# Kernel tuning notes

Hardware: AMD Instinct MI355X
Metric: run time of the kernel (lower is better)

## Reference

```python
import jax, jax.numpy as jnp
import numpy as np

N = 50000      # nodes
E = 800000     # edges
D = 256        # hidden_dim (input node features)
A = 128        # attention_dim = attention_ratio * heads
H = 8          # heads
DK = A // H    # 16


def setup_inputs() -> dict:
    key = jax.random.key(0)
    ks = jax.random.split(key, 6)
    x = jax.random.normal(ks[0], (N, D), dtype=jnp.float32)
    # small weight scale keeps exp(pre) well-conditioned (module uses tiny const init)
    Wq = jax.random.normal(ks[1], (A, D), dtype=jnp.float32) * 0.02
    bq = jnp.full((A,), 0.01, dtype=jnp.float32)
    Wk = jax.random.normal(ks[2], (A, D), dtype=jnp.float32) * 0.02
    bk = jnp.full((A,), 0.01, dtype=jnp.float32)
    edge_index = jax.random.randint(ks[3], (2, E), 0, N, dtype=jnp.int32)
    # d0_index[1] holds the two node indices each duplicated edge score scatters to
    d0_index = jax.random.randint(ks[4], (2, 2 * E), 0, N, dtype=jnp.int32)
    return {"x": x, "Wq": Wq, "bq": bq, "Wk": Wk, "bk": bk,
            "edge_index": edge_index, "d0_index": d0_index}


def reference(x, Wq, bq, Wk, bk, edge_index, d0_index):
    # linear projections -> [N, H, DK]
    q = (x @ Wq.T + bq).reshape(N, H, DK)
    k = (x @ Wk.T + bk).reshape(N, H, DK)
    src, dst = edge_index[0], edge_index[1]
    q_i = q[src]   # [E, H, DK]
    k_j = k[dst]
    q_j = q[dst]
    k_i = k[src]
    # symmetrized scaled-dot attention score per edge/head
    pre = 0.5 * jnp.sum(q_i * k_j + q_j * k_i, axis=-1)  # [E, H]
    pre = jnp.mean(pre, axis=-1)                          # [E]
    diagA1 = jnp.exp(pre)
    # duplicate each edge score: (a, a, b, b, ...) == torch (view(-1,1)*ones(E,2)).view(-1)
    edge_score_per_node = jnp.repeat(diagA1, 2)           # [2E]
    diagA0 = jax.ops.segment_sum(edge_score_per_node, d0_index[1], num_segments=N)
    return diagA0, diagA1
```

## Files before the change

kernel.cpp:

```cpp
#include <hip/hip_runtime.h>
#include <hip/hip_bf16.h>

#define N_NODES 50000
#define N_EDGES 800000
#define DIM 256
#define QKDIM 256
#define NB_T  391
#define NBLK_P 391
#define SLOT  32
#define CAPB  (NBLK_P * SLOT)
#define ITEMS (2 * N_EDGES)
#define IPB   4096
#define PROJ_BLOCKS 782

typedef __bf16 bfrag  __attribute__((ext_vector_type(8)));
typedef __bf16 bf4    __attribute__((ext_vector_type(4)));
typedef float  ffrag  __attribute__((ext_vector_type(4)));
typedef float  f2     __attribute__((ext_vector_type(2)));
typedef float  f4v    __attribute__((ext_vector_type(4)));

#define EP_PITCH 272

__global__ __launch_bounds__(256) void proj_bin(
    const float* __restrict__ x,
    const float* __restrict__ Wq, const float* __restrict__ Wk,
    const float* __restrict__ bq, const float* __restrict__ bk,
    unsigned char* __restrict__ qk8,
    const int* __restrict__ d0, unsigned int* __restrict__ rec,
    unsigned char* __restrict__ cnts)
{
    __shared__ unsigned char smem[32768];
    const int tid = threadIdx.x;

    if (blockIdx.x >= NBLK_P) {
        __bf16* As = (__bf16*)smem;
        const int wv   = tid >> 6;
        const int lane = tid & 63;
        const int m    = lane & 15;
        const int q    = lane >> 4;
        const int mbase = (blockIdx.x - NBLK_P) * 64;

        {
            const int srow = tid >> 2;
            const int c4   = tid & 3;
            int grow = mbase + srow;
            grow = grow < N_NODES ? grow : N_NODES - 1;
            const float* xp = x + (size_t)grow * DIM;
            const int mt_ = srow >> 4, m_ = srow & 15;
            #pragma unroll
            for (int i = 0; i < 16; ++i) {
                const int k = c4 * 4 + 16 * i;
                const f4v v = __builtin_nontemporal_load((const f4v*)(xp + k));
                bf4 o;
                o[0] = (__bf16)v[0]; o[1] = (__bf16)v[1];
                o[2] = (__bf16)v[2]; o[3] = (__bf16)v[3];
                const int seg = (k >> 5) * 4 + mt_;
                const int ln  = ((k >> 3) & 3) * 16 + m_;
                *(bf4*)(As + seg * 512 + ln * 8 + (k & 7)) = o;
            }
        }
        __syncthreads();

        ffrag acc[4][4] = {};

        #pragma unroll
        for (int h = 0; h < 2; ++h) {
            bfrag b[4][4];
            #pragma unroll
            for (int sp = 0; sp < 4; ++sp)
                #pragma unroll
                for (int nt = 0; nt < 4; ++nt) {
                    const int col = wv * 64 + nt * 16 + m;
                    const float* wrow = (col < 128)
                        ? (Wq + (size_t)col * DIM)
                        : (Wk + (size_t)(col - 128) * DIM);
                    const int k0 = 32 * (4 * h + sp) + 8 * q;
                    const float4 f0 = *(const float4*)(wrow + k0);
                    const float4 f1 = *(const float4*)(wrow + k0 + 4);
                    bfrag o;
                    o[0] = (__bf16)f0.x; o[1] = (__bf16)f0.y;
                    o[2] = (__bf16)f0.z; o[3] = (__bf16)f0.w;
                    o[4] = (__bf16)f1.x; o[5] = (__bf16)f1.y;
                    o[6] = (__bf16)f1.z; o[7] = (__bf16)f1.w;
                    b[sp][nt] = o;
                }
            #pragma unroll
            for (int sp = 0; sp < 4; ++sp) {
                bfrag a[4];
                #pragma unroll
                for (int mt = 0; mt < 4; ++mt)
                    a[mt] = *(const bfrag*)(As + ((4 * h + sp) * 4 + mt) * 512 + lane * 8);
                #pragma unroll
                for (int mt = 0; mt < 4; ++mt)
                    #pragma unroll
                    for (int nt = 0; nt < 4; ++nt)
                        acc[mt][nt] = __builtin_amdgcn_mfma_f32_16x16x32_bf16(
                                          a[mt], b[sp][nt], acc[mt][nt], 0, 0, 0);
            }
        }

        __syncthreads();
        unsigned char* ep = (unsigned char*)As;
        #pragma unroll
        for (int nt = 0; nt < 4; ++nt) {
            const int col  = wv * 64 + nt * 16 + m;
            const float bias = (col < 128) ? bq[col] : bk[col - 128];
            #pragma unroll
            for (int mt = 0; mt < 4; ++mt) {
                #pragma unroll
                for (int r = 0; r < 4; ++r) {
                    const int rl = mt * 16 + q * 4 + r;
                    const float v = acc[mt][nt][r] + bias;
                    const int pk = __builtin_amdgcn_cvt_pk_fp8_f32(v, v, 0, false);
                    ep[rl * EP_PITCH + col] = (unsigned char)(pk & 0xFF);
                }
            }
        }
        __syncthreads();
        {
            const int rl = tid >> 2;
            const int ch = tid & 3;
            const int grow = mbase + rl;
            if (grow < N_NODES) {
                const uint4* s4 = (const uint4*)(ep + rl * EP_PITCH + ch * 64);
                const uint4 t0 = s4[0], t1 = s4[1], t2 = s4[2], t3 = s4[3];
                uint4* g = (uint4*)(qk8 + (size_t)grow * QKDIM + ch * 64);
                g[0] = t0; g[1] = t1; g[2] = t2; g[3] = t3;
            }
        }
        return;
    }

    int* lcnt = (int*)smem;
    const int pb = blockIdx.x;

    for (int b = tid; b < NB_T; b += 256) lcnt[b] = 0;
    __syncthreads();
    const int base = pb * IPB;
    int tg[16];
    #pragma unroll
    for (int r = 0; r < 16; ++r) {
        const int i = base + r * 256 + tid;
        tg[r] = (i < ITEMS) ? d0[i] : -1;
        if (tg[r] >= 0) atomicAdd(&lcnt[tg[r] >> 7], 1);
    }
    __syncthreads();
    for (int b = tid; b < NB_T; b += 256) {
        const int c = lcnt[b];
        cnts[(size_t)pb * NB_T + b] = (unsigned char)(c < SLOT ? c : SLOT);
        lcnt[b] = 0;
    }
    __syncthreads();
    #pragma unroll
    for (int r = 0; r < 16; ++r) {
        if (tg[r] >= 0) {
            const int i = base + r * 256 + tid;
            const int b = tg[r] >> 7;
            const int off = atomicAdd(&lcnt[b], 1);
            if (off < SLOT)
                rec[(size_t)b * CAPB + pb * SLOT + off] =
                    ((unsigned int)(tg[r] & 127) << 20) | (unsigned int)(i >> 1);
        }
    }
}

__global__ __launch_bounds__(256) void edge_compute(
    const unsigned char* __restrict__ qk8,
    const int* __restrict__ edge_index,
    float* __restrict__ out)
{
    const int wave = (blockIdx.x * blockDim.x + threadIdx.x) >> 6;
    const int lane = threadIdx.x & 63;
    const int g = lane >> 2;
    const int j = lane & 3;
    const int e = wave * 16 + g;

    const int src = __builtin_nontemporal_load(edge_index + e);
    const int dst = __builtin_nontemporal_load(edge_index + N_EDGES + e);

    const uint4* rs = (const uint4*)(qk8 + (size_t)src * QKDIM);
    const uint4* rd = (const uint4*)(qk8 + (size_t)dst * QKDIM);

    uint4 a[4], b[4];
    #pragma unroll
    for (int i = 0; i < 4; ++i) a[i] = rs[4 * i + j];
    #pragma unroll
    for (int i = 0; i < 4; ++i) b[i] = rd[4 * ((i + 2) & 3) + j];

    f2 acc = {0.f, 0.f};
    #pragma unroll
    for (int i = 0; i < 4; ++i) {
        const unsigned int* ua = (const unsigned int*)&a[i];
        const unsigned int* ub = (const unsigned int*)&b[i];
        #pragma unroll
        for (int t = 0; t < 4; ++t) {
            const f2 x0 = __builtin_amdgcn_cvt_pk_f32_fp8(ua[t], false);
            const f2 y0 = __builtin_amdgcn_cvt_pk_f32_fp8(ub[t], false);
            const f2 x1 = __builtin_amdgcn_cvt_pk_f32_fp8(ua[t], true);
            const f2 y1 = __builtin_amdgcn_cvt_pk_f32_fp8(ub[t], true);
            acc += x0 * y0;
            acc += x1 * y1;
        }
    }
    float p = acc[0] + acc[1];
    p += __shfl_xor(p, 1, 64);
    p += __shfl_xor(p, 2, 64);

    if (j == 0)
        out[N_NODES + e] = __expf(p * 0.0625f);
}

__global__ __launch_bounds__(1024) void phase_scatter(
    const unsigned int* __restrict__ rec, const unsigned char* __restrict__ cnts,
    float* __restrict__ out)
{
    __shared__ float acc[16][128];
    __shared__ unsigned char lc[NBLK_P];
    const int b = blockIdx.x;
    const int tid = threadIdx.x;
    const int wid = tid >> 6;
    for (int i = tid; i < 16 * 128; i += 1024) ((float*)acc)[i] = 0.f;
    if (tid < NBLK_P) lc[tid] = cnts[(size_t)tid * NB_T + b];
    __syncthreads();

    const unsigned int* rb = rec + (size_t)b * CAPB;
    for (int s = tid; s < CAPB; s += 1024) {
        const int blk = s >> 5;
        const int off = s & (SLOT - 1);
        if (off < (int)lc[blk]) {
            const unsigned int r = rb[s];
            const float v = out[N_NODES + (r & 0xFFFFF)];
            atomicAdd(&acc[wid][r >> 20], v);
        }
    }
    __syncthreads();

    if (tid < 128) {
        float s = 0.f;
        #pragma unroll
        for (int w = 0; w < 16; ++w) s += acc[w][tid];
        const int n = b * 128 + tid;
        if (n < N_NODES) out[n] = s;
    }
}

__global__ __launch_bounds__(256) void edge_atomic(
    const unsigned char* __restrict__ qk8,
    const int* __restrict__ edge_index, const int* __restrict__ d0,
    float* __restrict__ out)
{
    const int wave = (blockIdx.x * blockDim.x + threadIdx.x) >> 6;
    const int lane = threadIdx.x & 63;
    const int g = lane >> 2, j = lane & 3;
    const int e = wave * 16 + g;

    const int src = edge_index[e];
    const int dst = edge_index[N_EDGES + e];

    const uint4* rs = (const uint4*)(qk8 + (size_t)src * QKDIM);
    const uint4* rd = (const uint4*)(qk8 + (size_t)dst * QKDIM);

    uint4 a[4], b[4];
    #pragma unroll
    for (int i = 0; i < 4; ++i) a[i] = rs[4 * i + j];
    #pragma unroll
    for (int i = 0; i < 4; ++i) b[i] = rd[4 * ((i + 2) & 3) + j];

    f2 acc = {0.f, 0.f};
    #pragma unroll
    for (int i = 0; i < 4; ++i) {
        const unsigned int* ua = (const unsigned int*)&a[i];
        const unsigned int* ub = (const unsigned int*)&b[i];
        #pragma unroll
        for (int t = 0; t < 4; ++t) {
            const f2 x0 = __builtin_amdgcn_cvt_pk_f32_fp8(ua[t], false);
            const f2 y0 = __builtin_amdgcn_cvt_pk_f32_fp8(ub[t], false);
            const f2 x1 = __builtin_amdgcn_cvt_pk_f32_fp8(ua[t], true);
            const f2 y1 = __builtin_amdgcn_cvt_pk_f32_fp8(ub[t], true);
            acc += x0 * y0;
            acc += x1 * y1;
        }
    }
    float p = acc[0] + acc[1];
    p += __shfl_xor(p, 1, 64);
    p += __shfl_xor(p, 2, 64);

    if (j < 2) {
        const float val = __expf(p * 0.0625f);
        if (j == 0) out[N_NODES + e] = val;
        atomicAdd(&out[d0[2 * e + j]], val);
    }
}


extern "C" void kernel_launch(void* const* d_in, const int* in_sizes, int n_in,
                              void* d_out, int out_size, void* d_ws, size_t ws_size,
                              hipStream_t stream) {
    const float* x  = (const float*)d_in[0];
    const float* Wq = (const float*)d_in[1];
    const float* bq = (const float*)d_in[2];
    const float* Wk = (const float*)d_in[3];
    const float* bk = (const float*)d_in[4];
    const int* edge_index = (const int*)d_in[5];
    const int* d0 = (const int*)d_in[6] + 2 * N_EDGES;
    float* out = (float*)d_out;

    char* w = (char*)d_ws;
    unsigned char* qk8 = (unsigned char*)w;  w += (size_t)N_NODES * QKDIM;
    unsigned int* rec = (unsigned int*)w;    w += (size_t)NB_T * CAPB * 4;
    unsigned char* cnts = (unsigned char*)w; w += (size_t)NBLK_P * NB_T;

    const size_t need = (size_t)(w - (char*)d_ws);
    const int use_bin = (ws_size >= need) ? 1 : 0;

    if (use_bin) {
        proj_bin<<<NBLK_P + PROJ_BLOCKS, 256, 0, stream>>>(
            x, Wq, Wk, bq, bk, qk8, d0, rec, cnts);
        edge_compute<<<N_EDGES / 64, 256, 0, stream>>>(qk8, edge_index, out);
        phase_scatter<<<NB_T, 1024, 0, stream>>>(rec, cnts, out);
    } else {
        hipMemsetAsync(out, 0, N_NODES * sizeof(float), stream);
        proj_bin<<<NBLK_P + PROJ_BLOCKS, 256, 0, stream>>>(
            x, Wq, Wk, bq, bk, qk8, d0, rec, cnts);
        edge_atomic<<<N_EDGES / 64, 256, 0, stream>>>(qk8, edge_index, d0, out);
    }
}
```

Before: 201.9 us.

## Shrink projection tile to 16 rows per block and load x directly into registers

The projection blocks now each handle 16 node rows instead of 64, so there are 3125 of them instead of 782. Each wave loads its x row and the W fragments straight from global memory into MFMA operands, with no LDS staging of x and one fewer barrier. This adds parallelism and cuts LDS use and per-block latency. In exchange, each W fragment is reused across far fewer rows, so W must be reloaded and reconverted four times as often; it should mostly hit in cache.

New measurement: 269.1 us. +33.3%, slower.

```diff
diff --git a/kernel.cpp b/kernel.cpp
--- a/kernel.cpp
+++ b/kernel.cpp
@@ -11,7 +11,7 @@
 #define CAPB  (NBLK_P * SLOT)
 #define ITEMS (2 * N_EDGES)
 #define IPB   4096
-#define PROJ_BLOCKS 782
+#define PROJ_BLOCKS 3125
 
 typedef __bf16 bfrag  __attribute__((ext_vector_type(8)));
 typedef __bf16 bf4    __attribute__((ext_vector_type(4)));
@@ -29,104 +29,72 @@
     const int* __restrict__ d0, unsigned int* __restrict__ rec,
     unsigned char* __restrict__ cnts)
 {
-    __shared__ unsigned char smem[32768];
+    __shared__ unsigned char smem[16 * EP_PITCH];
     const int tid = threadIdx.x;
 
     if (blockIdx.x >= NBLK_P) {
-        __bf16* As = (__bf16*)smem;
+        const int mb   = blockIdx.x - NBLK_P;
         const int wv   = tid >> 6;
         const int lane = tid & 63;
         const int m    = lane & 15;
         const int q    = lane >> 4;
-        const int mbase = (blockIdx.x - NBLK_P) * 64;
-
-        {
-            const int srow = tid >> 2;
-            const int c4   = tid & 3;
-            int grow = mbase + srow;
-            grow = grow < N_NODES ? grow : N_NODES - 1;
-            const float* xp = x + (size_t)grow * DIM;
-            const int mt_ = srow >> 4, m_ = srow & 15;
+        const int row  = mb * 16 + m;
+
+        const float* xrow = x + (size_t)row * DIM;
+
+        const float* wrow[4];
+        float bias[4];
+        #pragma unroll
+        for (int nt = 0; nt < 4; ++nt) {
+            const int col = wv * 64 + nt * 16 + m;
+            wrow[nt] = (col < 128) ? (Wq + (size_t)col * DIM)
+                                   : (Wk + (size_t)(col - 128) * DIM);
+            bias[nt] = (col < 128) ? bq[col] : bk[col - 128];
+        }
+
+        ffrag acc[4] = {};
+
+        #pragma unroll
+        for (int ks = 0; ks < 8; ++ks) {
+            const int k0 = ks * 32 + q * 8;
+            const float4 f0 = *(const float4*)(xrow + k0);
+            const float4 f1 = *(const float4*)(xrow + k0 + 4);
+            bfrag a;
+            a[0] = (__bf16)f0.x; a[1] = (__bf16)f0.y;
+            a[2] = (__bf16)f0.z; a[3] = (__bf16)f0.w;
+            a[4] = (__bf16)f1.x; a[5] = (__bf16)f1.y;
+            a[6] = (__bf16)f1.z; a[7] = (__bf16)f1.w;
             #pragma unroll
-            for (int i = 0; i < 16; ++i) {
-                const int k = c4 * 4 + 16 * i;
-                const f4v v = __builtin_nontemporal_load((const f4v*)(xp + k));
-                bf4 o;
-                o[0] = (__bf16)v[0]; o[1] = (__bf16)v[1];
-                o[2] = (__bf16)v[2]; o[3] = (__bf16)v[3];
-                const int seg = (k >> 5) * 4 + mt_;
-                const int ln  = ((k >> 3) & 3) * 16 + m_;
-                *(bf4*)(As + seg * 512 + ln * 8 + (k & 7)) = o;
+            for (int nt = 0; nt < 4; ++nt) {
+                const float4 g0 = *(const float4*)(wrow[nt] + k0);
+                const float4 g1 = *(const float4*)(wrow[nt] + k0 + 4);
+                bfrag b;
+                b[0] = (__bf16)g0.x; b[1] = (__bf16)g0.y;
+                b[2] = (__bf16)g0.z; b[3] = (__bf16)g0.w;
+                b[4] = (__bf16)g1.x; b[5] = (__bf16)g1.y;
+                b[6] = (__bf16)g1.z; b[7] = (__bf16)g1.w;
+                acc[nt] = __builtin_amdgcn_mfma_f32_16x16x32_bf16(a, b, acc[nt], 0, 0, 0);
             }
         }
-        __syncthreads();
-
-        ffrag acc[4][4] = {};
-
-        #pragma unroll
-        for (int h = 0; h < 2; ++h) {
-            bfrag b[4][4];
+
+        unsigned char* ep = smem;
+        #pragma unroll
+        for (int nt = 0; nt < 4; ++nt) {
+            const int col = wv * 64 + nt * 16 + m;
             #pragma unroll
-            for (int sp = 0; sp < 4; ++sp)
-                #pragma unroll
-                for (int nt = 0; nt < 4; ++nt) {
-                    const int col = wv * 64 + nt * 16 + m;
-                    const float* wrow = (col < 128)
-                        ? (Wq + (size_t)col * DIM)
-                        : (Wk + (size_t)(col - 128) * DIM);
-                    const int k0 = 32 * (4 * h + sp) + 8 * q;
-                    const float4 f0 = *(const float4*)(wrow + k0);
-                    const float4 f1 = *(const float4*)(wrow + k0 + 4);
-                    bfrag o;
-                    o[0] = (__bf16)f0.x; o[1] = (__bf16)f0.y;
-                    o[2] = (__bf16)f0.z; o[3] = (__bf16)f0.w;
-                    o[4] = (__bf16)f1.x; o[5] = (__bf16)f1.y;
-                    o[6] = (__bf16)f1.z; o[7] = (__bf16)f1.w;
-                    b[sp][nt] = o;
-                }
-            #pragma unroll
-            for (int sp = 0; sp < 4; ++sp) {
-                bfrag a[4];
-                #pragma unroll
-                for (int mt = 0; mt < 4; ++mt)
-                    a[mt] = *(const bfrag*)(As + ((4 * h + sp) * 4 + mt) * 512 + lane * 8);
-                #pragma unroll
-                for (int mt = 0; mt < 4; ++mt)
-                    #pragma unroll
-                    for (int nt = 0; nt < 4; ++nt)
-                        acc[mt][nt] = __builtin_amdgcn_mfma_f32_16x16x32_bf16(
-                                          a[mt], b[sp][nt], acc[mt][nt], 0, 0, 0);
-            }
-        }
-
-        __syncthreads();
-        unsigned char* ep = (unsigned char*)As;
-        #pragma unroll
-        for (int nt = 0; nt < 4; ++nt) {
-            const int col  = wv * 64 + nt * 16 + m;
-            const float bias = (col < 128) ? bq[col] : bk[col - 128];
-            #pragma unroll
-            for (int mt = 0; mt < 4; ++mt) {
-                #pragma unroll
-                for (int r = 0; r < 4; ++r) {
-                    const int rl = mt * 16 + q * 4 + r;
-                    const float v = acc[mt][nt][r] + bias;
-                    const int pk = __builtin_amdgcn_cvt_pk_fp8_f32(v, v, 0, false);
-                    ep[rl * EP_PITCH + col] = (unsigned char)(pk & 0xFF);
-                }
+            for (int r = 0; r < 4; ++r) {
+                const int rl = q * 4 + r;
+                const float v = acc[nt][r] + bias[nt];
+                const int pk = __builtin_amdgcn_cvt_pk_fp8_f32(v, v, 0, false);
+                ep[rl * EP_PITCH + col] = (unsigned char)(pk & 0xFF);
             }
         }
         __syncthreads();
         {
-            const int rl = tid >> 2;
-            const int ch = tid & 3;
-            const int grow = mbase + rl;
-            if (grow < N_NODES) {
-                const uint4* s4 = (const uint4*)(ep + rl * EP_PITCH + ch * 64);
-                const uint4 t0 = s4[0], t1 = s4[1], t2 = s4[2], t3 = s4[3];
-                uint4* g = (uint4*)(qk8 + (size_t)grow * QKDIM + ch * 64);
-                g[0] = t0; g[1] = t1; g[2] = t2; g[3] = t3;
-            }
+            const int rl = tid >> 4;
+            const int ch = tid & 15;
+            const uint4 t0 = *(const uint4*)(ep + rl * EP_PITCH + ch * 16);
+            *(uint4*)(qk8 + (size_t)(mb * 16 + rl) * QKDIM + ch * 16) = t0;
         }
         return;
     }
```
